# Optimization experiments

Hardware: AMD Instinct MI355X
Metric: run time of the kernel (lower is better)

Reference implementation:

```python
import jax, jax.numpy as jnp
import numpy as np

NEG_RATIO = 3.0
IOU_THR = 0.5
ALPHA = 1.0


def _cxcywh_to_xyxy(b):
    return jnp.concatenate([b[..., :2] - b[..., 2:] / 2, b[..., :2] + b[..., 2:] / 2], -1)


def _box_iou(a, b):  # a: [G,4] xyxy, b: [A,4] xyxy -> [G,A]
    lt = jnp.maximum(a[:, None, :2], b[None, :, :2])
    rb = jnp.minimum(a[:, None, 2:], b[None, :, 2:])
    wh = jnp.clip(rb - lt, 0.0)
    inter = wh[..., 0] * wh[..., 1]
    area_a = (a[:, 2] - a[:, 0]) * (a[:, 3] - a[:, 1])
    area_b = (b[:, 2] - b[:, 0]) * (b[:, 3] - b[:, 1])
    return inter / (area_a[:, None] + area_b[None, :] - inter)


def _encode(gt, anc):  # both cxcywh, last dim 4
    g_cxcy = (gt[..., :2] - anc[..., :2]) / anc[..., 2:]
    g_wh = jnp.log(gt[..., 2:]) - jnp.log(anc[..., 2:])
    return jnp.concatenate([g_cxcy, g_wh], -1)


def _match_one(boxes, labels, anchors):
    # boxes: [G,4] cxcywh, labels: [G] int, anchors: [A,4] cxcywh -> [A,5]
    ious = _box_iou(_cxcywh_to_xyxy(boxes), _cxcywh_to_xyxy(anchors))  # [G,A]
    best_gt_ov = ious.max(0)
    best_gt_idx = ious.argmax(0)  # [A]
    over = best_gt_ov > IOU_THR  # [A]
    lab_f = labels.astype(anchors.dtype)
    # anchors over threshold take their best gt, encoded w.r.t. that anchor
    enc_per_anchor = _encode(boxes[best_gt_idx], anchors)  # [A,4]
    ph = jnp.where(over[:, None],
                   jnp.concatenate([enc_per_anchor, lab_f[best_gt_idx][:, None]], -1),
                   0.0)  # [A,5]
    # every gt also claims its best anchor
    best_prior_idx = ious.argmax(1)  # [G]
    enc_best = _encode(boxes, anchors[best_prior_idx])  # [G,4]
    y2 = jnp.concatenate([enc_best, lab_f[:, None]], -1)
    return ph.at[best_prior_idx].set(y2)


def _multibox_loss(loc_pred, conf_pred, anchors, gt_boxes, gt_labels):
    B, A, C = conf_pred.shape
    target = jax.vmap(_match_one, in_axes=(0, 0, None))(gt_boxes, gt_labels, anchors)  # [B,A,5]
    pos = (target[:, :, 4:5] > 0).astype(loc_pred.dtype)  # [B,A,1]
    num_pos = pos.sum(axis=1, keepdims=True)  # [B,1,1]
    N = pos.sum()
    # smooth L1 on masked locations (beta=1), sum reduction
    d = pos * loc_pred - pos * target[:, :, :4]
    ad = jnp.abs(d)
    loc_loss = jnp.where(ad < 1.0, 0.5 * d * d, ad - 0.5).sum()
    # hard negative mining
    num_neg = jnp.minimum(NEG_RATIO * num_pos, A - 1)  # [B,1,1]
    lse = jax.scipy.special.logsumexp(conf_pred, axis=-1, keepdims=True)  # [B,A,1]
    idx01 = (target[:, :, 4:5] != 0).astype(jnp.int32)  # faithful: gathers class 0 or 1
    gathered = jnp.take_along_axis(conf_pred, idx01, axis=-1)  # [B,A,1]
    cls_l = (lse - gathered) * (1.0 - pos)  # zero-out positives
    order = jnp.argsort(-cls_l, axis=1)  # descending sort indices
    rank = jnp.argsort(order, axis=1)  # rank of each box's loss
    neg_mask = rank < num_neg
    sampled = jnp.logical_or(pos > 0, neg_mask)  # [B,A,1]
    s = sampled.astype(conf_pred.dtype)
    logits = (s * conf_pred).reshape(-1, C)
    labels_ce = (s * target[:, :, 4:5]).reshape(-1).astype(jnp.int32)
    lse2 = jax.scipy.special.logsumexp(logits, axis=-1)
    picked = jnp.take_along_axis(logits, labels_ce[:, None], axis=1)[:, 0]
    cls_loss = (lse2 - picked).sum()
    return (loc_loss + ALPHA * cls_loss) / N


def setup_inputs() -> dict:
    key = jax.random.key(0)
    k1, k2, k3, k4, k5, k6, k7 = jax.random.split(key, 7)
    B, A, C, G = 64, 8732, 81, 32
    loc_pred = jax.random.normal(k1, (B, A, 4), jnp.float32)
    conf_pred = jax.random.normal(k2, (B, A, C), jnp.float32)
    anc_cxcy = jax.random.uniform(k3, (A, 2), jnp.float32)
    anc_wh = jax.random.uniform(k4, (A, 2), jnp.float32) * 0.48 + 0.02
    anchors = jnp.concatenate([anc_cxcy, anc_wh], -1)
    gt_cxcy = jax.random.uniform(k5, (B, G, 2), jnp.float32) * 0.8 + 0.1
    gt_wh = jax.random.uniform(k6, (B, G, 2), jnp.float32) * 0.35 + 0.05
    gt_boxes = jnp.concatenate([gt_cxcy, gt_wh], -1)
    gt_labels = jax.random.randint(k7, (B, G), 0, C - 1, jnp.int32) + 1  # labels in 1..C-1
    return {"loc_pred": loc_pred, "conf_pred": conf_pred, "anchors": anchors,
            "gt_boxes": gt_boxes, "gt_labels": gt_labels}


def reference(loc_pred, conf_pred, anchors, gt_boxes, gt_labels):
    return _multibox_loss(loc_pred, conf_pred, anchors, gt_boxes, gt_labels)
```

## Files before the change

### kernel.cpp

```cpp
#include <hip/hip_runtime.h>
#include <math.h>

#pragma clang fp contract(off)

#define BB 64
#define AA 8732
#define CC 81
#define GG 32
#define AB (BB*AA)
#define A_BLOCKS 35
#define KC_BLOCKS 768
#define KA1_BLOCKS (BB*A_BLOCKS)
#define KA2_BLOCKS (BB*GG/4)
#define KC_STRIDE (KC_BLOCKS*256)


__global__ __launch_bounds__(256) void kAC(const float* __restrict__ anchors,
    const float* __restrict__ gt_boxes, const float* __restrict__ conf,
    unsigned char* __restrict__ bestg, unsigned int* __restrict__ bestp,
    float* __restrict__ cls_l)
{
    int tid = threadIdx.x;
    if (blockIdx.x < KC_BLOCKS) {
        const float4* __restrict__ src4 = (const float4*)conf;
        for (int r = blockIdx.x * 256 + tid; r < AB; r += KC_STRIDE) {
            int off = r * 81;
            int base4 = off >> 2;
            int pre = off & 3;
            float4 v[21];
#pragma unroll
            for (int j = 0; j < 21; ++j) v[j] = src4[(size_t)base4 + j];
            const float* f = (const float*)v;
            float s = 0.0f;
            s += (pre == 0) ? __expf(f[0]) : 0.0f;
            s += (pre <= 1) ? __expf(f[1]) : 0.0f;
            s += (pre <= 2) ? __expf(f[2]) : 0.0f;
#pragma unroll
            for (int k = 3; k <= 80; ++k) s += __expf(f[k]);
            s += (pre >= 1) ? __expf(f[81]) : 0.0f;
            s += (pre >= 2) ? __expf(f[82]) : 0.0f;
            s += (pre == 3) ? __expf(f[83]) : 0.0f;
            float r0 = (pre == 0) ? f[0] : (pre == 1) ? f[1] : (pre == 2) ? f[2] : f[3];
            cls_l[r] = __logf(s) - r0;
        }
    } else if (blockIdx.x < KC_BLOCKS + KA1_BLOCKS) {
        int blk = blockIdx.x - KC_BLOCKS;
        int b = blk / A_BLOCKS, ca = blk % A_BLOCKS;
        int a = ca * 256 + tid;
        __shared__ float4 gco[GG];
        __shared__ float gar[GG];
        if (tid < GG) {
            float4 gb = ((const float4*)gt_boxes)[b * GG + tid];
            float x1 = gb.x - gb.z / 2.0f, y1 = gb.y - gb.w / 2.0f;
            float x2 = gb.x + gb.z / 2.0f, y2 = gb.y + gb.w / 2.0f;
            gco[tid] = make_float4(x1, y1, x2, y2);
            gar[tid] = (x2 - x1) * (y2 - y1);
        }
        __syncthreads();
        if (a >= AA) return;
        float4 an = ((const float4*)anchors)[a];
        float ax1 = an.x - an.z / 2.0f, ay1 = an.y - an.w / 2.0f;
        float ax2 = an.x + an.z / 2.0f, ay2 = an.y + an.w / 2.0f;
        float aar = (ax2 - ax1) * (ay2 - ay1);
        float bi = -1.0f, bu = 1.0f; int bgi = 0;
#pragma unroll
        for (int g = 0; g < GG; ++g) {
            float4 c = gco[g];
            float ltx = fmaxf(c.x, ax1), lty = fmaxf(c.y, ay1);
            float rbx = fminf(c.z, ax2), rby = fminf(c.w, ay2);
            float w = fmaxf(rbx - ltx, 0.0f), h = fmaxf(rby - lty, 0.0f);
            float inter = w * h;
            float uni = gar[g] + aar - inter;
            if (inter * bu > bi * uni) { bi = inter; bu = uni; bgi = g; }
        }
        bestg[b * AA + a] = (2.0f * bi > bu) ? (unsigned char)bgi : (unsigned char)0xFF;
    } else {
        int wv = tid >> 6, lane = tid & 63;
        int pair = (blockIdx.x - KC_BLOCKS - KA1_BLOCKS) * 4 + wv;
        int b = pair >> 5, g = pair & 31;
        float4 gb = ((const float4*)gt_boxes)[b * GG + g];
        float gx1 = gb.x - gb.z / 2.0f, gy1 = gb.y - gb.w / 2.0f;
        float gx2 = gb.x + gb.z / 2.0f, gy2 = gb.y + gb.w / 2.0f;
        float gar = (gx2 - gx1) * (gy2 - gy1);
        float bi = -1.0f, bu = 1.0f; int ba = 0;
        for (int a = lane; a < AA; a += 64) {
            float4 an = ((const float4*)anchors)[a];
            float ax1 = an.x - an.z / 2.0f, ay1 = an.y - an.w / 2.0f;
            float ax2 = an.x + an.z / 2.0f, ay2 = an.y + an.w / 2.0f;
            float aar = (ax2 - ax1) * (ay2 - ay1);
            float ltx = fmaxf(gx1, ax1), lty = fmaxf(gy1, ay1);
            float rbx = fminf(gx2, ax2), rby = fminf(gy2, ay2);
            float w = fmaxf(rbx - ltx, 0.0f), h = fmaxf(rby - lty, 0.0f);
            float inter = w * h;
            float uni = gar + aar - inter;
            if (inter * bu > bi * uni) { bi = inter; bu = uni; ba = a; }
        }
#pragma unroll
        for (int off = 32; off > 0; off >>= 1) {
            float oi = __shfl_down(bi, off);
            float ou = __shfl_down(bu, off);
            int   oa = __shfl_down(ba, off);
            float p1 = oi * bu, p2 = bi * ou;
            bool take = (p1 > p2) || ((p1 == p2) && (oa < ba));
            if (take) { bi = oi; bu = ou; ba = oa; }
        }
        if (lane == 0) bestp[pair] = (unsigned int)ba;
    }
}

__global__ __launch_bounds__(256) void kB_finalize(const float* __restrict__ anchors,
    const float* __restrict__ gt_boxes, const int* __restrict__ gt_labels,
    const float* __restrict__ loc_pred,
    const unsigned char* __restrict__ bestg,
    const unsigned int* __restrict__ bestp,
    unsigned char* __restrict__ label_out,
    int* __restrict__ num_pos, double* __restrict__ loc_sum,
    unsigned int* __restrict__ ticket, double* __restrict__ btot_acc,
    int* __restrict__ np_acc)
{
    int b = blockIdx.x, tid = threadIdx.x;
    if (b == 0 && tid == 0) { *ticket = 0u; *btot_acc = 0.0; *np_acc = 0; }
    __shared__ int forced[AA];
    __shared__ float gcx[GG], gcy[GG], gw[GG], gh[GG];
    __shared__ int glab[GG];
    __shared__ double red_d[256];
    __shared__ int red_i[256];

    for (int i = tid; i < AA; i += 256) forced[i] = -1;
    if (tid < GG) {
        float4 gb = ((const float4*)gt_boxes)[b * GG + tid];
        gcx[tid] = gb.x; gcy[tid] = gb.y; gw[tid] = gb.z; gh[tid] = gb.w;
        glab[tid] = gt_labels[b * GG + tid];
    }
    __syncthreads();
    if (tid < GG) {
        int besta = (int)bestp[b * GG + tid];
        atomicMax(&forced[besta], tid);
    }
    __syncthreads();

    double lsum = 0.0; int pcount = 0;
    for (int a = tid; a < AA; a += 256) {
        int gf = forced[a];
        int gsel;
        if (gf >= 0) gsel = gf;
        else {
            unsigned char bg = bestg[b * AA + a];
            gsel = (bg == 0xFF) ? -1 : (int)bg;
        }
        int lab = 0;
        if (gsel >= 0) {
            lab = glab[gsel];
            float4 an = ((const float4*)anchors)[a];
            float e0 = (gcx[gsel] - an.x) / an.z;
            float e1 = (gcy[gsel] - an.y) / an.w;
            float e2 = logf(gw[gsel]) - logf(an.z);
            float e3 = logf(gh[gsel]) - logf(an.w);
            float4 lp = ((const float4*)loc_pred)[b * AA + a];
            float d0 = lp.x - e0, d1 = lp.y - e1, d2 = lp.z - e2, d3 = lp.w - e3;
            float t = 0.0f, ad;
            ad = fabsf(d0); t += (ad < 1.0f) ? 0.5f * d0 * d0 : ad - 0.5f;
            ad = fabsf(d1); t += (ad < 1.0f) ? 0.5f * d1 * d1 : ad - 0.5f;
            ad = fabsf(d2); t += (ad < 1.0f) ? 0.5f * d2 * d2 : ad - 0.5f;
            ad = fabsf(d3); t += (ad < 1.0f) ? 0.5f * d3 * d3 : ad - 0.5f;
            lsum += (double)t;
            pcount++;
        }
        label_out[b * AA + a] = (unsigned char)lab;
    }
    red_d[tid] = lsum; red_i[tid] = pcount;
    __syncthreads();
    for (int s = 128; s > 0; s >>= 1) {
        if (tid < s) { red_d[tid] += red_d[tid + s]; red_i[tid] += red_i[tid + s]; }
        __syncthreads();
    }
    if (tid == 0) { num_pos[b] = red_i[0]; loc_sum[b] = red_d[0]; }
}

__global__ __launch_bounds__(256) void kDE_select(const float* __restrict__ cls_l,
    const unsigned char* __restrict__ label, const float* __restrict__ conf,
    const int* __restrict__ num_pos, const double* __restrict__ loc_sum,
    unsigned int* __restrict__ ticket, double* __restrict__ btot_acc,
    int* __restrict__ np_acc, float* __restrict__ out)
{
    int b = blockIdx.x, tid = threadIdx.x;
    __shared__ unsigned int cl[AA];
    __shared__ unsigned int hist[256];
    __shared__ unsigned int sh_prefix, sh_remaining;
    __shared__ double red_d[256];
    __shared__ unsigned int red_u[256];
    __shared__ double sh_pos;

    const float* src = cls_l + b * AA;
    const unsigned char* lb = label + b * AA;
    double pc = 0.0;
    for (int i = tid; i < AA; i += 256) {
        int lab = lb[i];
        float v = fmaxf(src[i], 0.0f);
        if (lab > 0) {
            size_t rowb = (size_t)(b * AA + i) * 81;
            pc += (double)(src[i] + conf[rowb] - conf[rowb + lab]);
            cl[i] = 0u;
        } else {
            cl[i] = __float_as_uint(v);
        }
    }
    red_d[tid] = pc;
    __syncthreads();
    for (int s = 128; s > 0; s >>= 1) {
        if (tid < s) red_d[tid] += red_d[tid + s];
        __syncthreads();
    }
    if (tid == 0) sh_pos = red_d[0];

    int np_ = num_pos[b];
    int k = min(3 * np_, AA - 1);
    double topk = 0.0;
    int p_t_pos = 0;
    if (tid == 0) { sh_prefix = 0u; sh_remaining = (unsigned int)k; }
    __syncthreads();

    if (k > 0) {
        for (int shift = 24; shift >= 0; shift -= 8) {
            hist[tid] = 0u;
            __syncthreads();
            unsigned int mask = (shift == 24) ? 0u : (0xFFFFFFFFu << (shift + 8));
            unsigned int pre = sh_prefix;
            for (int i = tid; i < AA; i += 256) {
                unsigned int u = cl[i];
                if ((u & mask) == pre) atomicAdd(&hist[(u >> shift) & 255], 1u);
            }
            __syncthreads();
            if (tid < 64) {
                int l = tid;
                unsigned int h4 = hist[4 * l] + hist[4 * l + 1]
                                + hist[4 * l + 2] + hist[4 * l + 3];
                unsigned int S = h4;
#pragma unroll
                for (int off = 1; off < 64; off <<= 1) {
                    unsigned int o = __shfl_down(S, off);
                    S += (l + off < 64) ? o : 0u;
                }
                unsigned int rem = sh_remaining;
                unsigned long long ball = __ballot(S >= rem);
                int L = 63 - __clzll(ball);
                if (l == L) {
                    unsigned int rem2 = rem - (S - h4);
                    unsigned int c = 0;
                    for (int dd = 4 * L + 3; dd >= 4 * L; --dd) {
                        c += hist[dd];
                        if (c >= rem2) {
                            sh_prefix = pre | ((unsigned int)dd << shift);
                            sh_remaining = rem2 - (c - hist[dd]);
                            break;
                        }
                    }
                }
            }
            __syncthreads();
        }
        unsigned int vbits = sh_prefix;
        unsigned int myc = 0; double mys = 0.0;
        for (int i = tid; i < AA; i += 256) {
            unsigned int u = cl[i];
            if (u > vbits) { myc++; mys += (double)__uint_as_float(u); }
        }
        red_u[tid] = myc; red_d[tid] = mys;
        __syncthreads();
        for (int s2 = 128; s2 > 0; s2 >>= 1) {
            if (tid < s2) { red_u[tid] += red_u[tid + s2]; red_d[tid] += red_d[tid + s2]; }
            __syncthreads();
        }
        int cnt_gt = (int)red_u[0];
        double sum_gt = red_d[0];
        topk = sum_gt + (double)(k - cnt_gt) * (double)__uint_as_float(vbits);
        if (tid == 0 && vbits == 0u) {
            int t = k - cnt_gt, c2 = 0;
            for (int i = 0; i < AA && c2 < t; ++i) {
                if (cl[i] == 0u) { c2++; if (lb[i] > 0) p_t_pos++; }
            }
        }
    }
    if (tid == 0) {
        int unsampled = AA - np_ - k + p_t_pos;
        double clsb = sh_pos + topk + (double)unsampled * (double)logf(81.0f);
        double myb = loc_sum[b] + clsb;
        atomicAdd(btot_acc, myb);
        atomicAdd(np_acc, np_);
        __threadfence();
        unsigned int t = atomicAdd(ticket, 1u);
        if (t == BB - 1) {
            double tt = atomicAdd(btot_acc, 0.0);
            int nn = atomicAdd(np_acc, 0);
            out[0] = (float)(tt / (double)nn);
        }
    }
}

extern "C" void kernel_launch(void* const* d_in, const int* in_sizes, int n_in,
                              void* d_out, int out_size, void* d_ws, size_t ws_size,
                              hipStream_t stream) {
    (void)in_sizes; (void)n_in; (void)out_size; (void)ws_size;
    const float* loc_pred  = (const float*)d_in[0];
    const float* conf_pred = (const float*)d_in[1];
    const float* anchors   = (const float*)d_in[2];
    const float* gt_boxes  = (const float*)d_in[3];
    const int*   gt_labels = (const int*)d_in[4];

    char* ws = (char*)d_ws;
    unsigned int*  bestp    = (unsigned int*)(ws + 0);
    unsigned char* bestg    = (unsigned char*)(ws + 16640);
    unsigned char* label    = (unsigned char*)(ws + 575488);
    float*         cls_l    = (float*)(ws + 1134336);
    int*           num_pos  = (int*)(ws + 3369728);
    double*        loc_sum  = (double*)(ws + 3369984);
    unsigned int*  ticket   = (unsigned int*)(ws + 3370496);
    double*        btot_acc = (double*)(ws + 3370504);
    int*           np_acc   = (int*)(ws + 3370512);

    kAC       <<<KC_BLOCKS + KA1_BLOCKS + KA2_BLOCKS, 256, 0, stream>>>(
        anchors, gt_boxes, conf_pred, bestg, bestp, cls_l);
    kB_finalize<<<BB, 256, 0, stream>>>(anchors, gt_boxes, gt_labels, loc_pred,
        bestg, bestp, label, num_pos, loc_sum, ticket, btot_acc, np_acc);
    kDE_select<<<BB, 256, 0, stream>>>(cls_l, label, conf_pred, num_pos, loc_sum,
        ticket, btot_acc, np_acc, (float*)d_out);
}
```

Before: 371.2 us.

## Stage conf rows through LDS for logsumexp and fuse finalize with selection kernel

The logsumexp pass now loads 64 rows per block into shared memory with coalesced float4 loads, and four threads cooperate on each row, replacing per-thread strided 21-float4 register loads. The finalize and top-k selection kernels are merged into a single 1024-thread-per-batch kernel that keeps labels in shared memory. It also uses per-wave histograms and shuffle reductions to cut LDS atomic contention and sync steps. Only 64 blocks of 1024 threads run the fused stage, so the GPU is mostly idle during that phase, and shared memory per block grows.

```diff
diff --git a/kernel.cpp b/kernel.cpp
--- a/kernel.cpp
+++ b/kernel.cpp
@@ -7,48 +7,31 @@
 #define AA 8732
 #define CC 81
 #define GG 32
-#define AB (BB*AA)
 #define A_BLOCKS 35
-#define KC_BLOCKS 768
 #define KA1_BLOCKS (BB*A_BLOCKS)
 #define KA2_BLOCKS (BB*GG/4)
-#define KC_STRIDE (KC_BLOCKS*256)
+#define ROWS_PC 64
+#define KC_BLOCKS (BB*AA/ROWS_PC)
+#define CHUNK_F4 (ROWS_PC*81/4)
 
 
 __global__ __launch_bounds__(256) void kAC(const float* __restrict__ anchors,
     const float* __restrict__ gt_boxes, const float* __restrict__ conf,
     unsigned char* __restrict__ bestg, unsigned int* __restrict__ bestp,
-    float* __restrict__ cls_l)
+    float* __restrict__ cls_l, unsigned int* __restrict__ ticket,
+    double* __restrict__ btot_acc, int* __restrict__ np_acc)
 {
+    __shared__ float buf[ROWS_PC * 81];
     int tid = threadIdx.x;
-    if (blockIdx.x < KC_BLOCKS) {
-        const float4* __restrict__ src4 = (const float4*)conf;
-        for (int r = blockIdx.x * 256 + tid; r < AB; r += KC_STRIDE) {
-            int off = r * 81;
-            int base4 = off >> 2;
-            int pre = off & 3;
-            float4 v[21];
-#pragma unroll
-            for (int j = 0; j < 21; ++j) v[j] = src4[(size_t)base4 + j];
-            const float* f = (const float*)v;
-            float s = 0.0f;
-            s += (pre == 0) ? __expf(f[0]) : 0.0f;
-            s += (pre <= 1) ? __expf(f[1]) : 0.0f;
-            s += (pre <= 2) ? __expf(f[2]) : 0.0f;
-#pragma unroll
-            for (int k = 3; k <= 80; ++k) s += __expf(f[k]);
-            s += (pre >= 1) ? __expf(f[81]) : 0.0f;
-            s += (pre >= 2) ? __expf(f[82]) : 0.0f;
-            s += (pre == 3) ? __expf(f[83]) : 0.0f;
-            float r0 = (pre == 0) ? f[0] : (pre == 1) ? f[1] : (pre == 2) ? f[2] : f[3];
-            cls_l[r] = __logf(s) - r0;
-        }
-    } else if (blockIdx.x < KC_BLOCKS + KA1_BLOCKS) {
-        int blk = blockIdx.x - KC_BLOCKS;
+    if (blockIdx.x == 0 && tid == 0) {
+        *ticket = 0u; *btot_acc = 0.0; *np_acc = 0;
+    }
+    if (blockIdx.x < KA1_BLOCKS) {
+        int blk = blockIdx.x;
         int b = blk / A_BLOCKS, ca = blk % A_BLOCKS;
         int a = ca * 256 + tid;
-        __shared__ float4 gco[GG];
-        __shared__ float gar[GG];
+        float4* gco = (float4*)buf;
+        float* gar = buf + GG * 4;
         if (tid < GG) {
             float4 gb = ((const float4*)gt_boxes)[b * GG + tid];
             float x1 = gb.x - gb.z / 2.0f, y1 = gb.y - gb.w / 2.0f;
@@ -74,14 +57,14 @@
             if (inter * bu > bi * uni) { bi = inter; bu = uni; bgi = g; }
         }
         bestg[b * AA + a] = (2.0f * bi > bu) ? (unsigned char)bgi : (unsigned char)0xFF;
-    } else {
+    } else if (blockIdx.x < KA1_BLOCKS + KA2_BLOCKS) {
         int wv = tid >> 6, lane = tid & 63;
-        int pair = (blockIdx.x - KC_BLOCKS - KA1_BLOCKS) * 4 + wv;
+        int pair = (blockIdx.x - KA1_BLOCKS) * 4 + wv;
         int b = pair >> 5, g = pair & 31;
         float4 gb = ((const float4*)gt_boxes)[b * GG + g];
         float gx1 = gb.x - gb.z / 2.0f, gy1 = gb.y - gb.w / 2.0f;
         float gx2 = gb.x + gb.z / 2.0f, gy2 = gb.y + gb.w / 2.0f;
-        float gar = (gx2 - gx1) * (gy2 - gy1);
+        float gar2 = (gx2 - gx1) * (gy2 - gy1);
         float bi = -1.0f, bu = 1.0f; int ba = 0;
         for (int a = lane; a < AA; a += 64) {
             float4 an = ((const float4*)anchors)[a];
@@ -92,7 +75,7 @@
             float rbx = fminf(gx2, ax2), rby = fminf(gy2, ay2);
             float w = fmaxf(rbx - ltx, 0.0f), h = fmaxf(rby - lty, 0.0f);
             float inter = w * h;
-            float uni = gar + aar - inter;
+            float uni = gar2 + aar - inter;
             if (inter * bu > bi * uni) { bi = inter; bu = uni; ba = a; }
         }
 #pragma unroll
@@ -105,42 +88,65 @@
             if (take) { bi = oi; bu = ou; ba = oa; }
         }
         if (lane == 0) bestp[pair] = (unsigned int)ba;
+    } else {
+        int chunk = blockIdx.x - KA1_BLOCKS - KA2_BLOCKS;
+        const float4* __restrict__ src4 = (const float4*)conf;
+        size_t base4 = (size_t)chunk * CHUNK_F4;
+        float4* buf4 = (float4*)buf;
+#pragma unroll
+        for (int i = 0; i < 5; ++i) buf4[tid + 256 * i] = src4[base4 + tid + 256 * i];
+        if (tid < CHUNK_F4 - 1280) buf4[1280 + tid] = src4[base4 + 1280 + tid];
+        __syncthreads();
+        int r = tid >> 2, q = tid & 3;
+        const float* row = buf + r * 81;
+        int kstart = (q == 0) ? 0 : 21 + (q - 1) * 20;
+        float s = 0.0f;
+#pragma unroll
+        for (int k = 0; k < 20; ++k) s += __expf(row[kstart + k]);
+        if (q == 0) s += __expf(row[20]);
+        s += __shfl_xor(s, 1);
+        s += __shfl_xor(s, 2);
+        if (q == 0)
+            cls_l[chunk * ROWS_PC + r] = __logf(s) - row[0];
     }
 }
 
-__global__ __launch_bounds__(256) void kB_finalize(const float* __restrict__ anchors,
+__global__ __launch_bounds__(1024) void kBDE(const float* __restrict__ anchors,
     const float* __restrict__ gt_boxes, const int* __restrict__ gt_labels,
-    const float* __restrict__ loc_pred,
-    const unsigned char* __restrict__ bestg,
-    const unsigned int* __restrict__ bestp,
-    unsigned char* __restrict__ label_out,
-    int* __restrict__ num_pos, double* __restrict__ loc_sum,
-    unsigned int* __restrict__ ticket, double* __restrict__ btot_acc,
-    int* __restrict__ np_acc)
+    const float* __restrict__ loc_pred, const unsigned char* __restrict__ bestg,
+    const unsigned int* __restrict__ bestp, const float* __restrict__ cls_l,
+    const float* __restrict__ conf, unsigned int* __restrict__ ticket,
+    double* __restrict__ btot_acc, int* __restrict__ np_acc,
+    float* __restrict__ out)
 {
     int b = blockIdx.x, tid = threadIdx.x;
-    if (b == 0 && tid == 0) { *ticket = 0u; *btot_acc = 0.0; *np_acc = 0; }
     __shared__ int forced[AA];
+    __shared__ unsigned char slab[AA];
+    __shared__ unsigned int whist[16 * 256];
+    __shared__ unsigned int hist[256];
     __shared__ float gcx[GG], gcy[GG], gw[GG], gh[GG];
     __shared__ int glab[GG];
-    __shared__ double red_d[256];
-    __shared__ int red_i[256];
-
-    for (int i = tid; i < AA; i += 256) forced[i] = -1;
+    __shared__ double red_d[16];
+    __shared__ int red_i[16];
+    __shared__ unsigned int red_u[16];
+    __shared__ unsigned int sh_prefix, sh_remaining;
+    __shared__ int sh_np;
+    __shared__ double sh_loc;
+    unsigned int* cl = (unsigned int*)forced;
+
+    for (int i = tid; i < AA; i += 1024) forced[i] = -1;
     if (tid < GG) {
         float4 gb = ((const float4*)gt_boxes)[b * GG + tid];
         gcx[tid] = gb.x; gcy[tid] = gb.y; gw[tid] = gb.z; gh[tid] = gb.w;
         glab[tid] = gt_labels[b * GG + tid];
     }
     __syncthreads();
-    if (tid < GG) {
-        int besta = (int)bestp[b * GG + tid];
-        atomicMax(&forced[besta], tid);
-    }
+    if (tid < GG)
+        atomicMax(&forced[(int)bestp[b * GG + tid]], tid);
     __syncthreads();
 
     double lsum = 0.0; int pcount = 0;
-    for (int a = tid; a < AA; a += 256) {
+    for (int a = tid; a < AA; a += 1024) {
         int gf = forced[a];
         int gsel;
         if (gf >= 0) gsel = gf;
@@ -166,69 +172,67 @@
             lsum += (double)t;
             pcount++;
         }
-        label_out[b * AA + a] = (unsigned char)lab;
-    }
-    red_d[tid] = lsum; red_i[tid] = pcount;
-    __syncthreads();
-    for (int s = 128; s > 0; s >>= 1) {
-        if (tid < s) { red_d[tid] += red_d[tid + s]; red_i[tid] += red_i[tid + s]; }
-        __syncthreads();
-    }
-    if (tid == 0) { num_pos[b] = red_i[0]; loc_sum[b] = red_d[0]; }
-}
-
-__global__ __launch_bounds__(256) void kDE_select(const float* __restrict__ cls_l,
-    const unsigned char* __restrict__ label, const float* __restrict__ conf,
-    const int* __restrict__ num_pos, const double* __restrict__ loc_sum,
-    unsigned int* __restrict__ ticket, double* __restrict__ btot_acc,
-    int* __restrict__ np_acc, float* __restrict__ out)
-{
-    int b = blockIdx.x, tid = threadIdx.x;
-    __shared__ unsigned int cl[AA];
-    __shared__ unsigned int hist[256];
-    __shared__ unsigned int sh_prefix, sh_remaining;
-    __shared__ double red_d[256];
-    __shared__ unsigned int red_u[256];
-    __shared__ double sh_pos;
-
+        slab[a] = (unsigned char)lab;
+    }
+#pragma unroll
+    for (int off = 32; off > 0; off >>= 1) {
+        lsum += __shfl_down(lsum, off);
+        pcount += __shfl_down(pcount, off);
+    }
+    if ((tid & 63) == 0) { red_d[tid >> 6] = lsum; red_i[tid >> 6] = pcount; }
+    __syncthreads();
+    if (tid == 0) {
+        double L = 0.0; int P = 0;
+        for (int w = 0; w < 16; ++w) { L += red_d[w]; P += red_i[w]; }
+        sh_loc = L; sh_np = P;
+    }
+    __syncthreads();
+    int np_ = sh_np;
+
+    double pc = 0.0;
     const float* src = cls_l + b * AA;
-    const unsigned char* lb = label + b * AA;
-    double pc = 0.0;
-    for (int i = tid; i < AA; i += 256) {
-        int lab = lb[i];
-        float v = fmaxf(src[i], 0.0f);
+    for (int i = tid; i < AA; i += 1024) {
+        int lab = slab[i];
+        float sv = src[i];
         if (lab > 0) {
-            size_t rowb = (size_t)(b * AA + i) * 81;
-            pc += (double)(src[i] + conf[rowb] - conf[rowb + lab]);
+            size_t rowb = ((size_t)(b * AA + i)) * 81;
+            pc += (double)(sv + conf[rowb] - conf[rowb + lab]);
             cl[i] = 0u;
         } else {
-            cl[i] = __float_as_uint(v);
-        }
-    }
-    red_d[tid] = pc;
-    __syncthreads();
-    for (int s = 128; s > 0; s >>= 1) {
-        if (tid < s) red_d[tid] += red_d[tid + s];
-        __syncthreads();
-    }
-    if (tid == 0) sh_pos = red_d[0];
-
-    int np_ = num_pos[b];
+            cl[i] = __float_as_uint(fmaxf(sv, 0.0f));
+        }
+    }
+#pragma unroll
+    for (int off = 32; off > 0; off >>= 1) pc += __shfl_down(pc, off);
+    if ((tid & 63) == 0) red_d[tid >> 6] = pc;
+    __syncthreads();
+    double sum_pos = 0.0;
     int k = min(3 * np_, AA - 1);
+    if (tid == 0) {
+        for (int w = 0; w < 16; ++w) sum_pos += red_d[w];
+        sh_prefix = 0u; sh_remaining = (unsigned int)k;
+    }
+    __syncthreads();
+
     double topk = 0.0;
     int p_t_pos = 0;
-    if (tid == 0) { sh_prefix = 0u; sh_remaining = (unsigned int)k; }
-    __syncthreads();
-
     if (k > 0) {
         for (int shift = 24; shift >= 0; shift -= 8) {
-            hist[tid] = 0u;
+            for (int j = tid; j < 4096; j += 1024) whist[j] = 0u;
             __syncthreads();
             unsigned int mask = (shift == 24) ? 0u : (0xFFFFFFFFu << (shift + 8));
             unsigned int pre = sh_prefix;
-            for (int i = tid; i < AA; i += 256) {
+            unsigned int* myh = whist + (tid >> 6) * 256;
+            for (int i = tid; i < AA; i += 1024) {
                 unsigned int u = cl[i];
-                if ((u & mask) == pre) atomicAdd(&hist[(u >> shift) & 255], 1u);
+                if ((u & mask) == pre) atomicAdd(&myh[(u >> shift) & 255], 1u);
+            }
+            __syncthreads();
+            if (tid < 256) {
+                unsigned int t = 0;
+#pragma unroll
+                for (int w = 0; w < 16; ++w) t += whist[w * 256 + tid];
+                hist[tid] = t;
             }
             __syncthreads();
             if (tid < 64) {
@@ -261,30 +265,33 @@
         }
         unsigned int vbits = sh_prefix;
         unsigned int myc = 0; double mys = 0.0;
-        for (int i = tid; i < AA; i += 256) {
+        for (int i = tid; i < AA; i += 1024) {
             unsigned int u = cl[i];
             if (u > vbits) { myc++; mys += (double)__uint_as_float(u); }
         }
-        red_u[tid] = myc; red_d[tid] = mys;
+#pragma unroll
+        for (int off = 32; off > 0; off >>= 1) {
+            myc += __shfl_down(myc, off);
+            mys += __shfl_down(mys, off);
+        }
+        if ((tid & 63) == 0) { red_u[tid >> 6] = myc; red_d[tid >> 6] = mys; }
         __syncthreads();
-        for (int s2 = 128; s2 > 0; s2 >>= 1) {
-            if (tid < s2) { red_u[tid] += red_u[tid + s2]; red_d[tid] += red_d[tid + s2]; }
-            __syncthreads();
-        }
-        int cnt_gt = (int)red_u[0];
-        double sum_gt = red_d[0];
-        topk = sum_gt + (double)(k - cnt_gt) * (double)__uint_as_float(vbits);
-        if (tid == 0 && vbits == 0u) {
-            int t = k - cnt_gt, c2 = 0;
-            for (int i = 0; i < AA && c2 < t; ++i) {
-                if (cl[i] == 0u) { c2++; if (lb[i] > 0) p_t_pos++; }
+        if (tid == 0) {
+            unsigned int cnt_gt = 0; double sum_gt = 0.0;
+            for (int w = 0; w < 16; ++w) { cnt_gt += red_u[w]; sum_gt += red_d[w]; }
+            topk = sum_gt + (double)(k - (int)cnt_gt) * (double)__uint_as_float(vbits);
+            if (vbits == 0u) {
+                int t = k - (int)cnt_gt, c2 = 0;
+                for (int i = 0; i < AA && c2 < t; ++i) {
+                    if (cl[i] == 0u) { c2++; if (slab[i] > 0) p_t_pos++; }
+                }
             }
         }
     }
     if (tid == 0) {
         int unsampled = AA - np_ - k + p_t_pos;
-        double clsb = sh_pos + topk + (double)unsampled * (double)logf(81.0f);
-        double myb = loc_sum[b] + clsb;
+        double clsb = sum_pos + topk + (double)unsampled * (double)logf(81.0f);
+        double myb = sh_loc + clsb;
         atomicAdd(btot_acc, myb);
         atomicAdd(np_acc, np_);
         __threadfence();
@@ -309,19 +316,14 @@
 
     char* ws = (char*)d_ws;
     unsigned int*  bestp    = (unsigned int*)(ws + 0);
-    unsigned char* bestg    = (unsigned char*)(ws + 16640);
-    unsigned char* label    = (unsigned char*)(ws + 575488);
-    float*         cls_l    = (float*)(ws + 1134336);
-    int*           num_pos  = (int*)(ws + 3369728);
-    double*        loc_sum  = (double*)(ws + 3369984);
-    unsigned int*  ticket   = (unsigned int*)(ws + 3370496);
-    double*        btot_acc = (double*)(ws + 3370504);
-    int*           np_acc   = (int*)(ws + 3370512);
-
-    kAC       <<<KC_BLOCKS + KA1_BLOCKS + KA2_BLOCKS, 256, 0, stream>>>(
-        anchors, gt_boxes, conf_pred, bestg, bestp, cls_l);
-    kB_finalize<<<BB, 256, 0, stream>>>(anchors, gt_boxes, gt_labels, loc_pred,
-        bestg, bestp, label, num_pos, loc_sum, ticket, btot_acc, np_acc);
-    kDE_select<<<BB, 256, 0, stream>>>(cls_l, label, conf_pred, num_pos, loc_sum,
-        ticket, btot_acc, np_acc, (float*)d_out);
+    unsigned char* bestg    = (unsigned char*)(ws + 8192);
+    float*         cls_l    = (float*)(ws + 567040);
+    unsigned int*  ticket   = (unsigned int*)(ws + 2802432);
+    double*        btot_acc = (double*)(ws + 2802440);
+    int*           np_acc   = (int*)(ws + 2802448);
+
+    kAC <<<KA1_BLOCKS + KA2_BLOCKS + KC_BLOCKS, 256, 0, stream>>>(
+        anchors, gt_boxes, conf_pred, bestg, bestp, cls_l, ticket, btot_acc, np_acc);
+    kBDE<<<BB, 1024, 0, stream>>>(anchors, gt_boxes, gt_labels, loc_pred,
+        bestg, bestp, cls_l, conf_pred, ticket, btot_acc, np_acc, (float*)d_out);
 }
```

Result: faster. 323.4 us (-12.9%).
